# Kernel tuning notes

Measured on AMD Instinct MI355X. Metric: run time of the kernel, lower is better.

Reference implementation:

```python
import jax, jax.numpy as jnp
import numpy as np

HIDDEN = 1024
NUM_HEADS = 16
HEAD_SIZE = HIDDEN // NUM_HEADS


def setup_inputs() -> dict:
    key = jax.random.key(0)
    ks = jax.random.split(key, 5)
    B, S = 2, 2048
    x = jax.random.normal(ks[0], (B, S, HIDDEN), dtype=jnp.float32)
    # nn.Linear(hidden, 3*hidden): weight stored (in, out) for x @ W
    scale_qkv = 1.0 / np.sqrt(HIDDEN)
    w_qkv = jax.random.uniform(ks[1], (HIDDEN, 3 * HIDDEN), minval=-scale_qkv, maxval=scale_qkv, dtype=jnp.float32)
    b_qkv = jax.random.uniform(ks[2], (3 * HIDDEN,), minval=-scale_qkv, maxval=scale_qkv, dtype=jnp.float32)
    w_o = jax.random.uniform(ks[3], (HIDDEN, HIDDEN), minval=-scale_qkv, maxval=scale_qkv, dtype=jnp.float32)
    b_o = jax.random.uniform(ks[4], (HIDDEN,), minval=-scale_qkv, maxval=scale_qkv, dtype=jnp.float32)
    return {"x": x, "w_qkv": w_qkv, "b_qkv": b_qkv, "w_o": w_o, "b_o": b_o}


def reference(x, w_qkv, b_qkv, w_o, b_o):
    B, S, H = x.shape
    qkv = x @ w_qkv + b_qkv  # (B, S, 3H)
    q, k, v = jnp.split(qkv, 3, axis=-1)
    # (B, S, H) -> (B, nheads, S, head_size)
    def heads(t):
        return t.reshape(B, S, NUM_HEADS, HEAD_SIZE).transpose(0, 2, 1, 3)
    q, k, v = heads(q), heads(k), heads(v)
    scores = jnp.einsum('bhqd,bhkd->bhqk', q, k) / np.sqrt(HEAD_SIZE).astype(np.float32)
    causal = jnp.tril(jnp.ones((S, S), dtype=bool))  # k <= q
    scores = jnp.where(causal, scores, -jnp.inf)
    probs = jax.nn.softmax(scores, axis=-1)
    out = jnp.einsum('bhqk,bhkd->bqhd', probs, v).reshape(B, S, H)
    return out @ w_o + b_o
```

## Files before the change

### kernel.cpp

```cpp
#include <hip/hip_runtime.h>
#include <stdint.h>


typedef __bf16 bf16;
typedef __attribute__((ext_vector_type(8))) __bf16 bf16x8;
typedef __attribute__((ext_vector_type(4))) __bf16 bf16x4;
typedef __attribute__((ext_vector_type(4))) float floatx4;

#define SCL 0.18033688011112042f

__device__ __forceinline__ floatx4 mfma_bf16(bf16x8 a, bf16x8 b, floatx4 c) {
  return __builtin_amdgcn_mfma_f32_16x16x32_bf16(a, b, c, 0, 0, 0);
}

__device__ __forceinline__ void cp_g2l_16(const bf16* g, bf16* l) {
  __builtin_amdgcn_global_load_lds(
      (const __attribute__((address_space(1))) void*)g,
      (__attribute__((address_space(3))) void*)l, 16, 0, 0);
}

__global__ __launch_bounds__(256) void prep_kernel(
    const float* __restrict__ x, bf16* __restrict__ xb,
    const float* __restrict__ w_qkv, bf16* __restrict__ wqkvt,
    const float* __restrict__ w_o, bf16* __restrict__ wot) {
  const int b = blockIdx.x;
  const int tid = threadIdx.x;
  if (b < 4096) {
    const int i = (b * 256 + tid) * 4;
    floatx4 v = *(const floatx4*)(x + i);
    bf16x4 o;
    o[0] = (bf16)v[0]; o[1] = (bf16)v[1]; o[2] = (bf16)v[2]; o[3] = (bf16)v[3];
    *(bf16x4*)(xb + i) = o;
    return;
  }
  __shared__ float tile[32][33];
  const float* W; bf16* Wt; int K, N, n0, k0;
  if (b < 7168) {
    const int bb = b - 4096;
    W = w_qkv; Wt = wqkvt; K = 1024; N = 3072;
    n0 = (bb % 96) * 32; k0 = (bb / 96) * 32;
  } else {
    const int bb = b - 7168;
    W = w_o; Wt = wot; K = 1024; N = 1024;
    n0 = (bb & 31) * 32; k0 = (bb >> 5) * 32;
  }
  const int tx = tid & 31, ty = tid >> 5;
  for (int i = 0; i < 4; ++i)
    tile[ty + 8 * i][tx] = W[(size_t)(k0 + ty + 8 * i) * N + n0 + tx];
  __syncthreads();
  for (int i = 0; i < 4; ++i)
    Wt[(size_t)(n0 + ty + 8 * i) * K + k0 + tx] = (bf16)tile[tx][ty + 8 * i];
}

template <int MODE, int MI>
__global__ __launch_bounds__(256, 3) void gemm_bt_kernel(
    const bf16* __restrict__ A, const bf16* __restrict__ Bt,
    const float* __restrict__ bias, float* __restrict__ outF,
    bf16* __restrict__ qb, bf16* __restrict__ kb, bf16* __restrict__ vtb,
    int N, int K) {
  constexpr int BM = MI * 32;
  __shared__ bf16 As[BM * 32];
  __shared__ bf16 Bs[128 * 32];
  const int tid = threadIdx.x;
  const int w = tid >> 6, lane = tid & 63;
  const int l16 = lane & 15, quad = lane >> 4;
  const int m0 = blockIdx.y * BM, n0 = blockIdx.x * 128;
  const int wm = (w & 1) * (BM / 2), wn = (w >> 1) * 64;

  const int arow = w * (BM / 4) + (lane >> 2);
  const int acol = (lane & 3) * 8;
  const bf16* Ag = A + (size_t)(m0 + arow) * K + acol;
  bf16* Al = As + arow * 32 + acol;
  const int brow = w * 32 + (lane >> 2);
  const bf16* Bg = Bt + (size_t)(n0 + brow) * K + acol;
  bf16* Bl = Bs + brow * 32 + acol;

  floatx4 acc[MI][4];
#pragma unroll
  for (int i = 0; i < MI; ++i)
#pragma unroll
    for (int j = 0; j < 4; ++j) acc[i][j] = (floatx4){0.f, 0.f, 0.f, 0.f};

  for (int k0 = 0; k0 < K; k0 += 32) {
    __syncthreads();
    cp_g2l_16(Ag + k0, Al);
    if (MI == 4) cp_g2l_16(Ag + (size_t)16 * K + k0, Al + 16 * 32);
    cp_g2l_16(Bg + k0, Bl);
    cp_g2l_16(Bg + (size_t)16 * K + k0, Bl + 16 * 32);
    __syncthreads();
    bf16x8 af[MI], bfr[4];
#pragma unroll
    for (int i = 0; i < MI; ++i)
      af[i] = *(const bf16x8*)(&As[(wm + i * 16 + l16) * 32 + quad * 8]);
#pragma unroll
    for (int j = 0; j < 4; ++j)
      bfr[j] = *(const bf16x8*)(&Bs[(wn + j * 16 + l16) * 32 + quad * 8]);
#pragma unroll
    for (int i = 0; i < MI; ++i)
#pragma unroll
      for (int j = 0; j < 4; ++j)
        acc[i][j] = mfma_bf16(af[i], bfr[j], acc[i][j]);
  }

#pragma unroll
  for (int i = 0; i < MI; ++i)
#pragma unroll
    for (int j = 0; j < 4; ++j) {
      const int nn = n0 + wn + j * 16 + l16;
      const float bv = bias[nn];
      const int mbase = m0 + wm + i * 16 + quad * 4;
      if (MODE == 1) {
#pragma unroll
        for (int r = 0; r < 4; ++r)
          outF[(size_t)(mbase + r) * N + nn] = acc[i][j][r] + bv;
      } else {
        const int which = nn >> 10;
        const int rem = nn & 1023;
        const int h = rem >> 6, d = rem & 63;
        const int b = mbase >> 11, s = mbase & 2047;
        const size_t bh = (size_t)(b * 16 + h);
        if (which == 2) {
          bf16x4 pk;
#pragma unroll
          for (int r = 0; r < 4; ++r) pk[r] = (bf16)(acc[i][j][r] + bv);
          *(bf16x4*)(vtb + (bh * 64 + d) * 2048 + s) = pk;
        } else if (which == 0) {
#pragma unroll
          for (int r = 0; r < 4; ++r)
            qb[(bh * 2048 + s + r) * 64 + d] = (bf16)((acc[i][j][r] + bv) * SCL);
        } else {
#pragma unroll
          for (int r = 0; r < 4; ++r)
            kb[(bh * 2048 + s + r) * 64 + d] = (bf16)(acc[i][j][r] + bv);
        }
      }
    }
}

__global__ __launch_bounds__(256, 4) void attn_kernel(
    const bf16* __restrict__ Qb, const bf16* __restrict__ Kb,
    const bf16* __restrict__ Vtb, bf16* __restrict__ attnb) {
  __shared__ __align__(16) char smem[20480];
  const int bid = blockIdx.x;
  const int bh = (bid & 7) * 4 + ((bid >> 3) & 3);
  const int p = bid >> 5;
  const int tid = threadIdx.x;
  const int w = tid >> 6, lane = tid & 63;
  const int l16 = lane & 15, quad = lane >> 4;
  const int qt = (w & 2) ? (63 - p) : p;
  const int q0 = qt * 32;
  const int b = bh >> 4, h = bh & 15;
  const bf16* Qh = Qb + (size_t)bh * 2048 * 64;
  const bf16* Kh = Kb + (size_t)bh * 2048 * 64;
  const bf16* Vh = Vtb + (size_t)bh * 64 * 2048;
  bf16* Pw = (bf16*)smem + w * 2368;
  const int pw_wr = quad * 288 + (quad >> 1) * 16 + l16;
  const int pw_rd = l16 * 72 + (l16 >> 3) * 16 + quad * 8;

  const int tmax = qt >> 1;
  const int half = (tmax + 1) >> 1;
  const int t0 = (w & 1) ? half : 0;
  const int t1 = (w & 1) ? (tmax + 1) : half;

  bf16x8 qf[2][2];
#pragma unroll
  for (int mb = 0; mb < 2; ++mb)
#pragma unroll
    for (int kq = 0; kq < 2; ++kq)
      qf[mb][kq] = *(const bf16x8*)(Qh + (size_t)(q0 + mb * 16 + l16) * 64 +
                                    kq * 32 + quad * 8);
  bf16x8 ones;
#pragma unroll
  for (int j = 0; j < 8; ++j) ones[j] = (bf16)1.0f;

  floatx4 O[2][4], Ol[2];
#pragma unroll
  for (int mb = 0; mb < 2; ++mb) {
#pragma unroll
    for (int nd = 0; nd < 4; ++nd) O[mb][nd] = (floatx4){0.f, 0.f, 0.f, 0.f};
    Ol[mb] = (floatx4){0.f, 0.f, 0.f, 0.f};
  }

  for (int t = t0; t < t1; ++t) {
    const bool diag = (t == tmax);
    const bf16* Kt = Kh + (size_t)t * 64 * 64;
    const bf16* Vt = Vh + (size_t)t * 64;

    bf16x8 kf[4][2];
#pragma unroll
    for (int nk = 0; nk < 4; ++nk)
#pragma unroll
      for (int kq = 0; kq < 2; ++kq)
        kf[nk][kq] =
            *(const bf16x8*)(Kt + (nk * 16 + l16) * 64 + kq * 32 + quad * 8);

    {
      floatx4 sf[4];
#pragma unroll
      for (int nk = 0; nk < 4; ++nk) {
        floatx4 a = (floatx4){0.f, 0.f, 0.f, 0.f};
        a = mfma_bf16(qf[0][0], kf[nk][0], a);
        a = mfma_bf16(qf[0][1], kf[nk][1], a);
        sf[nk] = a;
      }
#pragma unroll
      for (int nk = 0; nk < 4; ++nk)
#pragma unroll
        for (int r = 0; r < 4; ++r) {
          float s = sf[nk][r];
          if (diag) {
            const int kc = t * 64 + nk * 16 + l16;
            const int qrow = q0 + quad * 4 + r;
            s = (kc <= qrow) ? s : -1e30f;
          }
          Pw[pw_wr + r * 72 + nk * 16] = (bf16)__builtin_amdgcn_exp2f(s);
        }
    }
    floatx4 sg[4];
#pragma unroll
    for (int nk = 0; nk < 4; ++nk) {
      floatx4 a = (floatx4){0.f, 0.f, 0.f, 0.f};
      a = mfma_bf16(qf[1][0], kf[nk][0], a);
      a = mfma_bf16(qf[1][1], kf[nk][1], a);
      sg[nk] = a;
    }
    bf16x8 vf[4][2];
#pragma unroll
    for (int nd = 0; nd < 4; ++nd)
#pragma unroll
      for (int kq = 0; kq < 2; ++kq)
        vf[nd][kq] =
            *(const bf16x8*)(Vt + (nd * 16 + l16) * 2048 + kq * 32 + quad * 8);
#pragma unroll
    for (int nk = 0; nk < 4; ++nk)
#pragma unroll
      for (int r = 0; r < 4; ++r) {
        float s = sg[nk][r];
        if (diag) {
          const int kc = t * 64 + nk * 16 + l16;
          const int qrow = q0 + 16 + quad * 4 + r;
          s = (kc <= qrow) ? s : -1e30f;
        }
        Pw[pw_wr + 1184 + r * 72 + nk * 16] = (bf16)__builtin_amdgcn_exp2f(s);
      }

#pragma unroll
    for (int mb = 0; mb < 2; ++mb) {
      bf16x8 pf[2];
      pf[0] = *(const bf16x8*)(&Pw[pw_rd + mb * 1184]);
      pf[1] = *(const bf16x8*)(&Pw[pw_rd + mb * 1184 + 32]);
#pragma unroll
      for (int nd = 0; nd < 4; ++nd) {
        floatx4 o = O[mb][nd];
        o = mfma_bf16(pf[0], vf[nd][0], o);
        o = mfma_bf16(pf[1], vf[nd][1], o);
        O[mb][nd] = o;
      }
      Ol[mb] = mfma_bf16(pf[0], ones, Ol[mb]);
      Ol[mb] = mfma_bf16(pf[1], ones, Ol[mb]);
    }
  }

  __syncthreads();
  float* Cb = (float*)smem + (w >> 1) * 2560;
  if (w & 1) {
#pragma unroll
    for (int mb = 0; mb < 2; ++mb) {
#pragma unroll
      for (int nd = 0; nd < 4; ++nd)
        *(floatx4*)(Cb + ((mb * 4 + nd) * 64 + lane) * 4) = O[mb][nd];
      *(floatx4*)(Cb + ((8 + mb) * 64 + lane) * 4) = Ol[mb];
    }
  }
  __syncthreads();
  if (!(w & 1)) {
#pragma unroll
    for (int mb = 0; mb < 2; ++mb) {
#pragma unroll
      for (int nd = 0; nd < 4; ++nd)
        O[mb][nd] += *(const floatx4*)(Cb + ((mb * 4 + nd) * 64 + lane) * 4);
      Ol[mb] += *(const floatx4*)(Cb + ((8 + mb) * 64 + lane) * 4);
    }
#pragma unroll
    for (int mb = 0; mb < 2; ++mb)
#pragma unroll
      for (int r = 0; r < 4; ++r) {
        const int qrow = q0 + mb * 16 + quad * 4 + r;
        const float inv = 1.f / Ol[mb][r];
#pragma unroll
        for (int nd = 0; nd < 4; ++nd)
          attnb[((size_t)(b * 2048 + qrow)) * 1024 + h * 64 + nd * 16 + l16] =
              (bf16)(O[mb][nd][r] * inv);
      }
  }
}

extern "C" void kernel_launch(void* const* d_in, const int* in_sizes, int n_in,
                              void* d_out, int out_size, void* d_ws, size_t ws_size,
                              hipStream_t stream) {
  const float* x     = (const float*)d_in[0];
  const float* w_qkv = (const float*)d_in[1];
  const float* b_qkv = (const float*)d_in[2];
  const float* w_o   = (const float*)d_in[3];
  const float* b_o   = (const float*)d_in[4];
  float* out = (float*)d_out;

  char* ws = (char*)d_ws;
  bf16* xb    = (bf16*)ws; ws += (size_t)4096 * 1024 * 2;
  bf16* wqkvt = (bf16*)ws; ws += (size_t)3072 * 1024 * 2;
  bf16* wot   = (bf16*)ws; ws += (size_t)1024 * 1024 * 2;
  bf16* qb    = (bf16*)ws; ws += (size_t)32 * 2048 * 64 * 2;
  bf16* kb    = (bf16*)ws; ws += (size_t)32 * 2048 * 64 * 2;
  bf16* vtb   = (bf16*)ws; ws += (size_t)32 * 2048 * 64 * 2;
  bf16* attnb = (bf16*)ws; ws += (size_t)4096 * 1024 * 2;

  prep_kernel<<<8192, 256, 0, stream>>>(x, xb, w_qkv, wqkvt, w_o, wot);
  gemm_bt_kernel<0, 4><<<dim3(24, 32), 256, 0, stream>>>(
      xb, wqkvt, b_qkv, nullptr, qb, kb, vtb, 3072, 1024);
  attn_kernel<<<1024, 256, 0, stream>>>(qb, kb, vtb, attnb);
  gemm_bt_kernel<1, 2><<<dim3(8, 64), 256, 0, stream>>>(
      attnb, wot, b_o, out, nullptr, nullptr, nullptr, 1024, 1024);
}
```

Measured before the change: 203.0 us.

## Give each attention block one query tile split four ways across KV tiles

The attention kernel now launches 2048 blocks, one 32-row query tile each, ordered longest-first. The four waves take KV tiles round-robin (t = w, w+4, ...) and combine partial O and row sums through LDS in a two-stage tree reduction. K fragments for the next tile are prefetched during the current iteration, and launch bounds drop to 3 blocks/SM to leave room for the extra registers. This targets load imbalance and latency, at the cost of more blocks, an extra reduction step and lower occupancy.

```diff
diff --git a/kernel.cpp b/kernel.cpp
--- a/kernel.cpp
+++ b/kernel.cpp
@@ -137,17 +137,16 @@
     }
 }
 
-__global__ __launch_bounds__(256, 4) void attn_kernel(
+__global__ __launch_bounds__(256, 3) void attn_kernel(
     const bf16* __restrict__ Qb, const bf16* __restrict__ Kb,
     const bf16* __restrict__ Vtb, bf16* __restrict__ attnb) {
   __shared__ __align__(16) char smem[20480];
   const int bid = blockIdx.x;
   const int bh = (bid & 7) * 4 + ((bid >> 3) & 3);
-  const int p = bid >> 5;
+  const int qt = 63 - (bid >> 5);
   const int tid = threadIdx.x;
   const int w = tid >> 6, lane = tid & 63;
   const int l16 = lane & 15, quad = lane >> 4;
-  const int qt = (w & 2) ? (63 - p) : p;
   const int q0 = qt * 32;
   const int b = bh >> 4, h = bh & 15;
   const bf16* Qh = Qb + (size_t)bh * 2048 * 64;
@@ -157,10 +156,8 @@
   const int pw_wr = quad * 288 + (quad >> 1) * 16 + l16;
   const int pw_rd = l16 * 72 + (l16 >> 3) * 16 + quad * 8;
 
-  const int tmax = qt >> 1;
-  const int half = (tmax + 1) >> 1;
-  const int t0 = (w & 1) ? half : 0;
-  const int t1 = (w & 1) ? (tmax + 1) : half;
+  const int nt = (qt >> 1) + 1;
+  const int tdiag = nt - 1;
 
   bf16x8 qf[2][2];
 #pragma unroll
@@ -181,18 +178,28 @@
     Ol[mb] = (floatx4){0.f, 0.f, 0.f, 0.f};
   }
 
-  for (int t = t0; t < t1; ++t) {
-    const bool diag = (t == tmax);
-    const bf16* Kt = Kh + (size_t)t * 64 * 64;
-    const bf16* Vt = Vh + (size_t)t * 64;
-
-    bf16x8 kf[4][2];
+  bf16x8 kf[4][2];
+  {
+    const bf16* Kt = Kh + (size_t)(w < nt ? w : 0) * 64 * 64;
 #pragma unroll
     for (int nk = 0; nk < 4; ++nk)
 #pragma unroll
       for (int kq = 0; kq < 2; ++kq)
         kf[nk][kq] =
             *(const bf16x8*)(Kt + (nk * 16 + l16) * 64 + kq * 32 + quad * 8);
+  }
+
+  for (int t = w; t < nt; t += 4) {
+    const bool diag = (t == tdiag);
+    const bf16* Vt = Vh + (size_t)t * 64;
+
+    bf16x8 vf[4][2];
+#pragma unroll
+    for (int nd = 0; nd < 4; ++nd)
+#pragma unroll
+      for (int kq = 0; kq < 2; ++kq)
+        vf[nd][kq] =
+            *(const bf16x8*)(Vt + (nd * 16 + l16) * 2048 + kq * 32 + quad * 8);
 
     {
       floatx4 sf[4];
@@ -224,13 +231,16 @@
       a = mfma_bf16(qf[1][1], kf[nk][1], a);
       sg[nk] = a;
     }
-    bf16x8 vf[4][2];
-#pragma unroll
-    for (int nd = 0; nd < 4; ++nd)
-#pragma unroll
-      for (int kq = 0; kq < 2; ++kq)
-        vf[nd][kq] =
-            *(const bf16x8*)(Vt + (nd * 16 + l16) * 2048 + kq * 32 + quad * 8);
+    {
+      const int tn = (t + 4 < nt) ? (t + 4) : 0;
+      const bf16* Kt = Kh + (size_t)tn * 64 * 64;
+#pragma unroll
+      for (int nk = 0; nk < 4; ++nk)
+#pragma unroll
+        for (int kq = 0; kq < 2; ++kq)
+          kf[nk][kq] =
+              *(const bf16x8*)(Kt + (nk * 16 + l16) * 64 + kq * 32 + quad * 8);
+    }
 #pragma unroll
     for (int nk = 0; nk < 4; ++nk)
 #pragma unroll
@@ -261,9 +271,31 @@
     }
   }
 
-  __syncthreads();
-  float* Cb = (float*)smem + (w >> 1) * 2560;
-  if (w & 1) {
+  float* Cb = (float*)smem;
+  __syncthreads();
+  if (w >= 2) {
+    float* S = Cb + (w - 2) * 2560;
+#pragma unroll
+    for (int mb = 0; mb < 2; ++mb) {
+#pragma unroll
+      for (int nd = 0; nd < 4; ++nd)
+        *(floatx4*)(S + ((mb * 4 + nd) * 64 + lane) * 4) = O[mb][nd];
+      *(floatx4*)(S + ((8 + mb) * 64 + lane) * 4) = Ol[mb];
+    }
+  }
+  __syncthreads();
+  if (w < 2) {
+    const float* S = Cb + w * 2560;
+#pragma unroll
+    for (int mb = 0; mb < 2; ++mb) {
+#pragma unroll
+      for (int nd = 0; nd < 4; ++nd)
+        O[mb][nd] += *(const floatx4*)(S + ((mb * 4 + nd) * 64 + lane) * 4);
+      Ol[mb] += *(const floatx4*)(S + ((8 + mb) * 64 + lane) * 4);
+    }
+  }
+  __syncthreads();
+  if (w == 1) {
 #pragma unroll
     for (int mb = 0; mb < 2; ++mb) {
 #pragma unroll
@@ -273,7 +305,7 @@
     }
   }
   __syncthreads();
-  if (!(w & 1)) {
+  if (w == 0) {
 #pragma unroll
     for (int mb = 0; mb < 2; ++mb) {
 #pragma unroll
@@ -317,7 +349,7 @@
   prep_kernel<<<8192, 256, 0, stream>>>(x, xb, w_qkv, wqkvt, w_o, wot);
   gemm_bt_kernel<0, 4><<<dim3(24, 32), 256, 0, stream>>>(
       xb, wqkvt, b_qkv, nullptr, qb, kb, vtb, 3072, 1024);
-  attn_kernel<<<1024, 256, 0, stream>>>(qb, kb, vtb, attnb);
+  attn_kernel<<<2048, 256, 0, stream>>>(qb, kb, vtb, attnb);
   gemm_bt_kernel<1, 2><<<dim3(8, 64), 256, 0, stream>>>(
       attnb, wot, b_o, out, nullptr, nullptr, nullptr, 1024, 1024);
 }
```

New measurement: 210.9 us. 3.9% more time.

## Share K/V tiles through swizzled LDS across four query waves in attention

Applied to the files above, without the earlier changes.

Restructures the attention kernel so each block owns a 128-row query block, split into four waves of 32 rows. Each K/V tile is staged once into LDS with async global-to-LDS copies using an XOR-style swizzle, and all four waves read it from there instead of loading it from global memory per wave. The old split of the key range across wave pairs, and the LDS reduction that merged their partial results, are removed. The grid is halved, occupancy is lowered to 3 blocks, and two block barriers are added per tile. Waves whose causal range ends earlier sit idle at those barriers, and blocks now carry unequal causal work since the old pairing of short and long query tiles is gone.

```diff
diff --git a/kernel.cpp b/kernel.cpp
--- a/kernel.cpp
+++ b/kernel.cpp
@@ -137,30 +137,37 @@
     }
 }
 
-__global__ __launch_bounds__(256, 4) void attn_kernel(
+__global__ __launch_bounds__(256, 3) void attn_kernel(
     const bf16* __restrict__ Qb, const bf16* __restrict__ Kb,
     const bf16* __restrict__ Vtb, bf16* __restrict__ attnb) {
-  __shared__ __align__(16) char smem[20480];
+  __shared__ bf16 Ks[4096];
+  __shared__ bf16 Vs[4096];
+  __shared__ bf16 Ps[4 * 2368];
   const int bid = blockIdx.x;
   const int bh = (bid & 7) * 4 + ((bid >> 3) & 3);
-  const int p = bid >> 5;
+  const int qblk = 15 - (bid >> 5);
   const int tid = threadIdx.x;
   const int w = tid >> 6, lane = tid & 63;
   const int l16 = lane & 15, quad = lane >> 4;
-  const int qt = (w & 2) ? (63 - p) : p;
-  const int q0 = qt * 32;
+  const int q0 = qblk * 128 + w * 32;
   const int b = bh >> 4, h = bh & 15;
   const bf16* Qh = Qb + (size_t)bh * 2048 * 64;
   const bf16* Kh = Kb + (size_t)bh * 2048 * 64;
   const bf16* Vh = Vtb + (size_t)bh * 64 * 2048;
-  bf16* Pw = (bf16*)smem + w * 2368;
+  bf16* Pw = Ps + w * 2368;
   const int pw_wr = quad * 288 + (quad >> 1) * 16 + l16;
   const int pw_rd = l16 * 72 + (l16 >> 3) * 16 + quad * 8;
 
-  const int tmax = qt >> 1;
-  const int half = (tmax + 1) >> 1;
-  const int t0 = (w & 1) ? half : 0;
-  const int t1 = (w & 1) ? (tmax + 1) : half;
+  const int nt = 2 * qblk + 2;
+  const int wdiag = q0 >> 6;
+
+  const int c0 = tid, c1 = 256 + tid;
+  const int ksrc0 = (c0 >> 3) * 64 + (((c0 & 7) - (c0 >> 3)) & 7) * 8;
+  const int ksrc1 = (c1 >> 3) * 64 + (((c1 & 7) - (c1 >> 3)) & 7) * 8;
+  const int vsrc0 = (c0 >> 3) * 2048 + (((c0 & 7) - (c0 >> 3)) & 7) * 8;
+  const int vsrc1 = (c1 >> 3) * 2048 + (((c1 & 7) - (c1 >> 3)) & 7) * 8;
+  bf16* kdst0 = Ks + c0 * 8; bf16* kdst1 = Ks + c1 * 8;
+  bf16* vdst0 = Vs + c0 * 8; bf16* vdst1 = Vs + c1 * 8;
 
   bf16x8 qf[2][2];
 #pragma unroll
@@ -181,18 +188,30 @@
     Ol[mb] = (floatx4){0.f, 0.f, 0.f, 0.f};
   }
 
-  for (int t = t0; t < t1; ++t) {
-    const bool diag = (t == tmax);
-    const bf16* Kt = Kh + (size_t)t * 64 * 64;
-    const bf16* Vt = Vh + (size_t)t * 64;
+  for (int t = 0; t < nt; ++t) {
+    __syncthreads();
+    {
+      const bf16* KtG = Kh + (size_t)t * 4096;
+      const bf16* VtG = Vh + t * 64;
+      cp_g2l_16(KtG + ksrc0, kdst0);
+      cp_g2l_16(KtG + ksrc1, kdst1);
+      cp_g2l_16(VtG + vsrc0, vdst0);
+      cp_g2l_16(VtG + vsrc1, vdst1);
+    }
+    __syncthreads();
+
+    if (t > wdiag) continue;
+    const bool diag = (t == wdiag);
 
     bf16x8 kf[4][2];
 #pragma unroll
     for (int nk = 0; nk < 4; ++nk)
 #pragma unroll
-      for (int kq = 0; kq < 2; ++kq)
-        kf[nk][kq] =
-            *(const bf16x8*)(Kt + (nk * 16 + l16) * 64 + kq * 32 + quad * 8);
+      for (int kq = 0; kq < 2; ++kq) {
+        const int row = nk * 16 + l16;
+        kf[nk][kq] = *(const bf16x8*)(
+            &Ks[row * 64 + ((kq * 4 + quad + row) & 7) * 8]);
+      }
 
     {
       floatx4 sf[4];
@@ -228,9 +247,11 @@
 #pragma unroll
     for (int nd = 0; nd < 4; ++nd)
 #pragma unroll
-      for (int kq = 0; kq < 2; ++kq)
-        vf[nd][kq] =
-            *(const bf16x8*)(Vt + (nd * 16 + l16) * 2048 + kq * 32 + quad * 8);
+      for (int kq = 0; kq < 2; ++kq) {
+        const int row = nd * 16 + l16;
+        vf[nd][kq] = *(const bf16x8*)(
+            &Vs[row * 64 + ((kq * 4 + quad + row) & 7) * 8]);
+      }
 #pragma unroll
     for (int nk = 0; nk < 4; ++nk)
 #pragma unroll
@@ -261,38 +282,17 @@
     }
   }
 
-  __syncthreads();
-  float* Cb = (float*)smem + (w >> 1) * 2560;
-  if (w & 1) {
-#pragma unroll
-    for (int mb = 0; mb < 2; ++mb) {
+#pragma unroll
+  for (int mb = 0; mb < 2; ++mb)
+#pragma unroll
+    for (int r = 0; r < 4; ++r) {
+      const int qrow = q0 + mb * 16 + quad * 4 + r;
+      const float inv = 1.f / Ol[mb][r];
 #pragma unroll
       for (int nd = 0; nd < 4; ++nd)
-        *(floatx4*)(Cb + ((mb * 4 + nd) * 64 + lane) * 4) = O[mb][nd];
-      *(floatx4*)(Cb + ((8 + mb) * 64 + lane) * 4) = Ol[mb];
-    }
-  }
-  __syncthreads();
-  if (!(w & 1)) {
-#pragma unroll
-    for (int mb = 0; mb < 2; ++mb) {
-#pragma unroll
-      for (int nd = 0; nd < 4; ++nd)
-        O[mb][nd] += *(const floatx4*)(Cb + ((mb * 4 + nd) * 64 + lane) * 4);
-      Ol[mb] += *(const floatx4*)(Cb + ((8 + mb) * 64 + lane) * 4);
-    }
-#pragma unroll
-    for (int mb = 0; mb < 2; ++mb)
-#pragma unroll
-      for (int r = 0; r < 4; ++r) {
-        const int qrow = q0 + mb * 16 + quad * 4 + r;
-        const float inv = 1.f / Ol[mb][r];
-#pragma unroll
-        for (int nd = 0; nd < 4; ++nd)
-          attnb[((size_t)(b * 2048 + qrow)) * 1024 + h * 64 + nd * 16 + l16] =
-              (bf16)(O[mb][nd][r] * inv);
-      }
-  }
+        attnb[((size_t)(b * 2048 + qrow)) * 1024 + h * 64 + nd * 16 + l16] =
+            (bf16)(O[mb][nd][r] * inv);
+    }
 }
 
 extern "C" void kernel_launch(void* const* d_in, const int* in_sizes, int n_in,
@@ -317,7 +317,7 @@
   prep_kernel<<<8192, 256, 0, stream>>>(x, xb, w_qkv, wqkvt, w_o, wot);
   gemm_bt_kernel<0, 4><<<dim3(24, 32), 256, 0, stream>>>(
       xb, wqkvt, b_qkv, nullptr, qb, kb, vtb, 3072, 1024);
-  attn_kernel<<<1024, 256, 0, stream>>>(qb, kb, vtb, attnb);
+  attn_kernel<<<512, 256, 0, stream>>>(qb, kb, vtb, attnb);
   gemm_bt_kernel<1, 2><<<dim3(8, 64), 256, 0, stream>>>(
       attnb, wot, b_o, out, nullptr, nullptr, nullptr, 1024, 1024);
 }
```

New measurement: 189.1 us. 6.8% less time.
